# Kernel tuning notes

Hardware: AMD Instinct MI355X
Metric: run time of the kernel (lower is better)

Reference implementation:

```python
import jax, jax.numpy as jnp
import numpy as np

N = 8192
N_DIM = 7
N_WIDTH = 64


def setup_inputs() -> dict:
    key = jax.random.key(0)
    ks = jax.random.split(key, 12)
    scale = 0.05
    u = lambda k, shape: scale * (2.0 * jax.random.uniform(k, shape) - 1.0)
    # Linear params stored as (in, out) so forward uses x @ W + b (same math as torch Linear).
    lin = lambda k, fan_in, fan_out: (
        jax.random.uniform(jax.random.fold_in(k, 0), (fan_in, fan_out),
                           minval=-1.0, maxval=1.0) / np.sqrt(fan_in),
        jax.random.uniform(jax.random.fold_in(k, 1), (fan_out,),
                           minval=-1.0, maxval=1.0) / np.sqrt(fan_in),
    )
    W1, b1 = lin(ks[1], N_DIM, N_WIDTH)
    W2, b2 = lin(ks[2], N_WIDTH, N_WIDTH)
    Wl, bl = lin(ks[3], N_WIDTH, 1)
    return {
        "x": jax.random.normal(ks[0], (N, N_DIM), dtype=jnp.float32),
        "alpha": jax.random.uniform(ks[4], (1,)),          # Edges.alpha = 1 * rand(1)
        "W1": W1, "b1": b1, "wt1": u(ks[5], (N_WIDTH, N_WIDTH)), "bs1": u(ks[6], (1,)),
        "W2": W2, "b2": b2, "wt2": u(ks[7], (N_WIDTH, N_WIDTH)), "bs2": u(ks[8], (1,)),
        "Wl": Wl, "bl": bl,
    }


def _edges(x, alpha):
    eta, phi = x[:, 1], x[:, 2]
    deta = eta[:, None] - eta[None, :]                      # (n, n)
    dphi = jnp.abs(phi[:, None] - phi[None, :])
    dphi = jnp.where(dphi > jnp.pi, 2.0 * jnp.pi - dphi, dphi)
    dRdR = deta * deta + dphi * dphi
    A = jnp.exp(-alpha[0] * dRdR)
    return jax.nn.softmax(A, axis=1) + jnp.eye(x.shape[0], dtype=x.dtype)


def _gcn_layer(X, A, W, b, wt, bs):
    X = jax.nn.relu(X @ W + b)                              # embed + relu
    X = (A @ X) @ wt + bs[0]                                # aggregate + mix + scalar bias
    return jax.nn.relu(X)


def reference(x, alpha, W1, b1, wt1, bs1, W2, b2, wt2, bs2, Wl, bl):
    A = _edges(x, alpha)
    V = jax.nn.relu(_gcn_layer(x, A, W1, b1, wt1, bs1))
    V = jax.nn.relu(_gcn_layer(V, A, W2, b2, wt2, bs2))
    s = V.sum(axis=0)                                       # (n_width,)
    return jax.nn.sigmoid(s @ Wl + bl)                      # (1,)
```

## Files before the change

kernel.cpp:

```cpp
#include <hip/hip_runtime.h>
#include <math.h>

#define NN 8192
#define L2E 1.44269504088896340736f
#define TWO_PI 6.28318530717958647693f

typedef _Float16 h8 __attribute__((ext_vector_type(8)));
typedef _Float16 h4 __attribute__((ext_vector_type(4)));
typedef float f32x4 __attribute__((ext_vector_type(4)));
typedef float f32x2 __attribute__((ext_vector_type(2)));
#define MFMA16(A, B, C) __builtin_amdgcn_mfma_f32_16x16x32_f16(A, B, C, 0, 0, 0)

#define GLD_LDS16(gsrc, ldst)                                          \
  __builtin_amdgcn_global_load_lds(                                    \
      (const __attribute__((address_space(1))) unsigned int*)(gsrc),   \
      (__attribute__((address_space(3))) unsigned int*)(ldst), 16, 0, 0)

union V8 { float4 v[2]; float f[8]; };

__global__ __launch_bounds__(256) void prep_kernel(
    const float* __restrict__ x, const float* __restrict__ alpha,
    const float* __restrict__ W1, const float* __restrict__ b1,
    float* __restrict__ eta_s, float* __restrict__ phi_s,
    float* __restrict__ H1, _Float16* __restrict__ HT1,
    float* __restrict__ svec)
{
  __shared__ float sW[448];
  __shared__ float sb[64];
  __shared__ float T[32][68];
  const int t = threadIdx.x;
  if (blockIdx.x == 0 && t < 64) svec[t] = 0.f;
  for (int k = t; k < 448; k += 256) sW[k] = W1[k];
  if (t < 64) sb[t] = b1[t];
  const float s = sqrtf(alpha[0] * L2E);
  const int i0 = blockIdx.x * 32;
  const int r = t >> 3, q = t & 7;
  const int i = i0 + r;
  float xv[7];
#pragma unroll
  for (int k = 0; k < 7; k++) xv[k] = x[i * 7 + k];
  if (q == 0) { eta_s[i] = xv[1] * s; phi_s[i] = xv[2] * s; }
  __syncthreads();
#pragma unroll
  for (int c = 0; c < 8; c++) {
    const int n = q * 8 + c;
    float hv = sb[n];
#pragma unroll
    for (int k = 0; k < 7; k++) hv = fmaf(xv[k], sW[k * 64 + n], hv);
    T[r][n] = fmaxf(hv, 0.f);
  }
  __syncthreads();
  for (int e = t; e < 512; e += 256)
    *(f32x4*)(H1 + (size_t)i0 * 64 + (e << 2)) =
        *(const f32x4*)&T[e >> 4][(e << 2) & 63];
  const int n = t >> 2, sg = (t & 3) * 8;
  h8 v;
#pragma unroll
  for (int ss = 0; ss < 8; ss++) v[ss] = (_Float16)T[sg + ss][n];
  *(h8*)(HT1 + (size_t)n * NN + i0 + sg) = v;
}

template <bool NEED_L>
__global__ __launch_bounds__(256, 4) void attn_pass(
    const float* __restrict__ eta_s, const float* __restrict__ phi_s,
    const _Float16* __restrict__ HT, const float* __restrict__ alpha,
    float* __restrict__ Ypart, float* __restrict__ lpart)
{
  __shared__ __align__(16) char smem[32768];
  const int tid = threadIdx.x;
  const int w = tid >> 6, lane = tid & 63, m = lane & 15, g = lane >> 4;
  const int tile = blockIdx.x >> 2, part = blockIdx.x & 3;
  const int i0 = tile << 5;
  const int jbase = part << 11;
  const float Cs = TWO_PI * sqrtf(alpha[0] * L2E);
  const float et0 = eta_s[i0 + m],      ph0 = phi_s[i0 + m];
  const float et1 = eta_s[i0 + 16 + m], ph1 = phi_s[i0 + 16 + m];

  const int joff = jbase + (w << 5) + (g << 3);
  const _Float16* hb = HT + (size_t)m * NN + joff;
  const float* ep = eta_s + joff;
  const float* pp = phi_s + joff;

  char* const slab = smem + (w << 13);

  f32x4 a00 = {0,0,0,0}, a01 = {0,0,0,0}, a02 = {0,0,0,0}, a03 = {0,0,0,0};
  f32x4 a10 = {0,0,0,0}, a11 = {0,0,0,0}, a12 = {0,0,0,0}, a13 = {0,0,0,0};
  f32x4 l0a = {0,0,0,0}, l1a = {0,0,0,0};
  const h8 onesv = {(_Float16)1.f, (_Float16)1.f, (_Float16)1.f, (_Float16)1.f,
                    (_Float16)1.f, (_Float16)1.f, (_Float16)1.f, (_Float16)1.f};

  V8 Eb[2], Pb[2];

#pragma unroll
  for (int k = 0; k < 4; ++k)
    GLD_LDS16(hb + (size_t)k * 16 * NN, slab + (k << 10));
  Eb[0].v[0] = *(const float4*)(ep);     Eb[0].v[1] = *(const float4*)(ep + 4);
  Pb[0].v[0] = *(const float4*)(pp);     Pb[0].v[1] = *(const float4*)(pp + 4);
  __builtin_amdgcn_sched_barrier(0);

  union AF { h8 v; decltype(__builtin_amdgcn_cvt_pkrtz(0.f, 0.f)) p[4]; };

#pragma unroll
  for (int s = 0; s < 16; ++s) {
    if (s < 15) {
      char* const nb = slab + (((s + 1) & 1) << 12);
      const _Float16* src = hb + (s + 1) * 128;
#pragma unroll
      for (int k = 0; k < 4; ++k)
        GLD_LDS16(src + (size_t)k * 16 * NN, nb + (k << 10));
      Eb[(s + 1) & 1].v[0] = *(const float4*)(ep + (s + 1) * 128);
      Eb[(s + 1) & 1].v[1] = *(const float4*)(ep + (s + 1) * 128 + 4);
      Pb[(s + 1) & 1].v[0] = *(const float4*)(pp + (s + 1) * 128);
      Pb[(s + 1) & 1].v[1] = *(const float4*)(pp + (s + 1) * 128 + 4);
    }
    __builtin_amdgcn_sched_barrier(0);
    if (s < 15) asm volatile("s_waitcnt vmcnt(8)" ::: "memory");
    else        asm volatile("s_waitcnt vmcnt(0)" ::: "memory");
    __builtin_amdgcn_sched_barrier(0);

    const char* fb = slab + ((s & 1) << 12) + (lane << 4);
    const h8 b0 = *(const h8*)(fb);
    const h8 b1 = *(const h8*)(fb + 1024);
    const h8 b2 = *(const h8*)(fb + 2048);
    const h8 b3 = *(const h8*)(fb + 3072);
    const V8& E = Eb[s & 1];
    const V8& P = Pb[s & 1];

    AF af0, af1;
#pragma unroll
    for (int tt = 0; tt < 8; tt += 2) {
      const f32x2 pj = {P.f[tt], P.f[tt + 1]};
      const f32x2 ej = {E.f[tt], E.f[tt + 1]};
      const f32x2 dp0 = ph0 - pj, dp1 = ph1 - pj;
      const f32x2 ad0 = {fabsf(dp0.x), fabsf(dp0.y)};
      const f32x2 ad1 = {fabsf(dp1.x), fabsf(dp1.y)};
      const f32x2 cm0 = Cs - ad0, cm1 = Cs - ad1;
      const f32x2 wr0 = {fminf(ad0.x, cm0.x), fminf(ad0.y, cm0.y)};
      const f32x2 wr1 = {fminf(ad1.x, cm1.x), fminf(ad1.y, cm1.y)};
      const f32x2 de0 = et0 - ej, de1 = et1 - ej;
      const f32x2 r20 = de0 * de0 + wr0 * wr0;
      const f32x2 r21 = de1 * de1 + wr1 * wr1;
      const f32x2 ax0 = {__builtin_amdgcn_exp2f(-r20.x),
                         __builtin_amdgcn_exp2f(-r20.y)};
      const f32x2 ax1 = {__builtin_amdgcn_exp2f(-r21.x),
                         __builtin_amdgcn_exp2f(-r21.y)};
      const f32x2 ga0 = ax0 * L2E - L2E;
      const f32x2 ga1 = ax1 * L2E - L2E;
      af0.p[tt >> 1] = __builtin_amdgcn_cvt_pkrtz(
          __builtin_amdgcn_exp2f(ga0.x), __builtin_amdgcn_exp2f(ga0.y));
      af1.p[tt >> 1] = __builtin_amdgcn_cvt_pkrtz(
          __builtin_amdgcn_exp2f(ga1.x), __builtin_amdgcn_exp2f(ga1.y));
    }
    a00 = MFMA16(af0.v, b0, a00); a01 = MFMA16(af0.v, b1, a01);
    a02 = MFMA16(af0.v, b2, a02); a03 = MFMA16(af0.v, b3, a03);
    a10 = MFMA16(af1.v, b0, a10); a11 = MFMA16(af1.v, b1, a11);
    a12 = MFMA16(af1.v, b2, a12); a13 = MFMA16(af1.v, b3, a13);
    if constexpr (NEED_L) {
      l0a = MFMA16(af0.v, onesv, l0a);
      l1a = MFMA16(af1.v, onesv, l1a);
    }
  }

  __syncthreads();

  typedef float Red2[32][66];
  Red2* red = (Red2*)smem;
  const int h = w >> 1;
  if ((w & 1) == 0) {
#pragma unroll
    for (int r = 0; r < 4; ++r) {
      red[h][g * 4 + r][m]      = a00[r]; red[h][g * 4 + r][16 + m] = a01[r];
      red[h][g * 4 + r][32 + m] = a02[r]; red[h][g * 4 + r][48 + m] = a03[r];
      red[h][16 + g * 4 + r][m]      = a10[r]; red[h][16 + g * 4 + r][16 + m] = a11[r];
      red[h][16 + g * 4 + r][32 + m] = a12[r]; red[h][16 + g * 4 + r][48 + m] = a13[r];
    }
    if constexpr (NEED_L) {
      if (m == 0) {
#pragma unroll
        for (int r = 0; r < 4; ++r) {
          red[h][g * 4 + r][64]      = l0a[r];
          red[h][16 + g * 4 + r][64] = l1a[r];
        }
      }
    }
  }
  __syncthreads();
  if (w & 1) {
#pragma unroll
    for (int r = 0; r < 4; ++r) {
      red[h][g * 4 + r][m]      += a00[r]; red[h][g * 4 + r][16 + m] += a01[r];
      red[h][g * 4 + r][32 + m] += a02[r]; red[h][g * 4 + r][48 + m] += a03[r];
      red[h][16 + g * 4 + r][m]      += a10[r]; red[h][16 + g * 4 + r][16 + m] += a11[r];
      red[h][16 + g * 4 + r][32 + m] += a12[r]; red[h][16 + g * 4 + r][48 + m] += a13[r];
    }
    if constexpr (NEED_L) {
      if (m == 0) {
#pragma unroll
        for (int r = 0; r < 4; ++r) {
          red[h][g * 4 + r][64]      += l0a[r];
          red[h][16 + g * 4 + r][64] += l1a[r];
        }
      }
    }
  }
  __syncthreads();
#pragma unroll
  for (int k = 0; k < 8; ++k) {
    const int e = tid + k * 256;
    Ypart[((size_t)part * NN + i0 + (e >> 6)) * 64 + (e & 63)] =
        red[0][e >> 6][e & 63] + red[1][e >> 6][e & 63];
  }
  if constexpr (NEED_L) {
    if (tid < 32)
      lpart[(size_t)part * NN + i0 + tid] = red[0][tid][64] + red[1][tid][64];
  }
}

__global__ __launch_bounds__(256) void mid_kernel(
    const float* __restrict__ Yp, const float* __restrict__ lp,
    const float* __restrict__ H1, const float* __restrict__ wt1,
    const float* __restrict__ bs1, const float* __restrict__ W2,
    const float* __restrict__ b2, float* __restrict__ H2,
    _Float16* __restrict__ HT2)
{
  __shared__ float sA[64][68];
  __shared__ float sB[64][68];
  __shared__ float U[16][68];
  __shared__ float sb2v[64];
  const int t = threadIdx.x;
  for (int e = t; e < 1024; e += 256) {
    const int rr = e >> 4, cc = (e << 2) & 63;
    *(f32x4*)&sA[rr][cc] = *(const f32x4*)(wt1 + (e << 2));
    *(f32x4*)&sB[rr][cc] = *(const f32x4*)(W2 + (e << 2));
  }
  if (t < 64) sb2v[t] = b2[t];
  const float bsv = bs1[0];
  const int i0 = blockIdx.x * 16;
  const int r = t >> 4, q = t & 15;
  const int i = i0 + r;
  float l = 0.f;
#pragma unroll
  for (int p = 0; p < 4; ++p) l += lp[(size_t)p * NN + i];
  const float rl = 1.0f / l;
  f32x4 ya = {0, 0, 0, 0};
#pragma unroll
  for (int p = 0; p < 4; ++p)
    ya += *(const f32x4*)(Yp + ((size_t)p * NN + i) * 64 + q * 4);
  const f32x4 h1 = *(const f32x4*)(H1 + (size_t)i * 64 + q * 4);
#pragma unroll
  for (int c = 0; c < 4; ++c) U[r][q * 4 + c] = fmaf(ya[c], rl, h1[c]);
  __syncthreads();
  float z[4];
#pragma unroll
  for (int c = 0; c < 4; ++c) z[c] = bsv;
#pragma unroll
  for (int k4 = 0; k4 < 64; k4 += 4) {
    const f32x4 u4 = *(const f32x4*)&U[r][k4];
#pragma unroll
    for (int kk = 0; kk < 4; ++kk) {
      const f32x4 sa = *(const f32x4*)&sA[k4 + kk][q * 4];
#pragma unroll
      for (int c = 0; c < 4; ++c) z[c] = fmaf(u4[kk], sa[c], z[c]);
    }
  }
  __syncthreads();
#pragma unroll
  for (int c = 0; c < 4; ++c) U[r][q * 4 + c] = fmaxf(z[c], 0.f);
  __syncthreads();
  float hv[4];
#pragma unroll
  for (int c = 0; c < 4; ++c) hv[c] = sb2v[q * 4 + c];
#pragma unroll
  for (int k4 = 0; k4 < 64; k4 += 4) {
    const f32x4 u4 = *(const f32x4*)&U[r][k4];
#pragma unroll
    for (int kk = 0; kk < 4; ++kk) {
      const f32x4 sb4 = *(const f32x4*)&sB[k4 + kk][q * 4];
#pragma unroll
      for (int c = 0; c < 4; ++c) hv[c] = fmaf(u4[kk], sb4[c], hv[c]);
    }
  }
  __syncthreads();
#pragma unroll
  for (int c = 0; c < 4; ++c) U[r][q * 4 + c] = fmaxf(hv[c], 0.f);
  __syncthreads();
  *(f32x4*)(H2 + (size_t)i0 * 64 + (t << 2)) =
      *(const f32x4*)&U[t >> 4][(t << 2) & 63];
  const int n = t >> 2, sg = (t & 3) * 4;
  h4 v;
#pragma unroll
  for (int ss = 0; ss < 4; ss++) v[ss] = (_Float16)U[sg + ss][n];
  *(h4*)(HT2 + (size_t)n * NN + i0 + sg) = v;
}

__global__ __launch_bounds__(256) void final_kernel(
    const float* __restrict__ Yp, const float* __restrict__ lp,
    const float* __restrict__ H2, const float* __restrict__ wt2,
    const float* __restrict__ bs2, float* __restrict__ svec)
{
  __shared__ float sA[64][68];
  __shared__ float U[16][68];
  __shared__ float cred[4][64];
  const int t = threadIdx.x;
  for (int e = t; e < 1024; e += 256) {
    const int rr = e >> 4, cc = (e << 2) & 63;
    *(f32x4*)&sA[rr][cc] = *(const f32x4*)(wt2 + (e << 2));
  }
  const float bsv = bs2[0];
  const int i0 = blockIdx.x * 16;
  const int r = t >> 4, q = t & 15;
  const int i = i0 + r;
  float l = 0.f;
#pragma unroll
  for (int p = 0; p < 4; ++p) l += lp[(size_t)p * NN + i];
  const float rl = 1.0f / l;
  f32x4 ya = {0, 0, 0, 0};
#pragma unroll
  for (int p = 0; p < 4; ++p)
    ya += *(const f32x4*)(Yp + ((size_t)p * NN + i) * 64 + q * 4);
  const f32x4 h2 = *(const f32x4*)(H2 + (size_t)i * 64 + q * 4);
#pragma unroll
  for (int c = 0; c < 4; ++c) U[r][q * 4 + c] = fmaf(ya[c], rl, h2[c]);
  __syncthreads();
  float z[4];
#pragma unroll
  for (int c = 0; c < 4; ++c) z[c] = bsv;
#pragma unroll
  for (int k4 = 0; k4 < 64; k4 += 4) {
    const f32x4 u4 = *(const f32x4*)&U[r][k4];
#pragma unroll
    for (int kk = 0; kk < 4; ++kk) {
      const f32x4 sa = *(const f32x4*)&sA[k4 + kk][q * 4];
#pragma unroll
      for (int c = 0; c < 4; ++c) z[c] = fmaf(u4[kk], sa[c], z[c]);
    }
  }
  __syncthreads();
#pragma unroll
  for (int c = 0; c < 4; ++c) U[r][q * 4 + c] = fmaxf(z[c], 0.f);
  __syncthreads();
  const int col = t & 63, rg = t >> 6;
  float ps = 0.f;
#pragma unroll
  for (int rr = 0; rr < 4; rr++) ps += U[rg * 4 + rr][col];
  cred[rg][col] = ps;
  __syncthreads();
  if (t < 64)
    atomicAdd(svec + t, cred[0][t] + cred[1][t] + cred[2][t] + cred[3][t]);
}

__global__ void out_kernel(const float* __restrict__ svec,
                           const float* __restrict__ Wl,
                           const float* __restrict__ bl,
                           float* __restrict__ out)
{
  const int t = threadIdx.x;
  float v = svec[t] * Wl[t];
#pragma unroll
  for (int off = 32; off > 0; off >>= 1) v += __shfl_down(v, off);
  if (t == 0) {
    const float logit = v + bl[0];
    out[0] = 1.0f / (1.0f + __builtin_amdgcn_exp2f(-logit * L2E));
  }
}

extern "C" void kernel_launch(void* const* d_in, const int* in_sizes, int n_in,
                              void* d_out, int out_size, void* d_ws,
                              size_t ws_size, hipStream_t stream)
{
  const float* x     = (const float*)d_in[0];
  const float* alpha = (const float*)d_in[1];
  const float* W1    = (const float*)d_in[2];
  const float* b1    = (const float*)d_in[3];
  const float* wt1   = (const float*)d_in[4];
  const float* bs1   = (const float*)d_in[5];
  const float* W2    = (const float*)d_in[6];
  const float* b2    = (const float*)d_in[7];
  const float* wt2   = (const float*)d_in[8];
  const float* bs2   = (const float*)d_in[9];
  const float* Wl    = (const float*)d_in[10];
  const float* bl    = (const float*)d_in[11];
  float* out = (float*)d_out;

  char* ws = (char*)d_ws;
  size_t off = 0;
  auto alloc = [&](size_t bytes) {
    void* p = ws + off;
    off = (off + bytes + 255) & ~(size_t)255;
    return p;
  };
  float* eta_s = (float*)alloc(NN * 4 + 256);
  float* phi_s = (float*)alloc(NN * 4 + 256);
  float* H1    = (float*)alloc((size_t)NN * 64 * 4);
  float* H2    = (float*)alloc((size_t)NN * 64 * 4);
  float* Ypart = (float*)alloc((size_t)4 * NN * 64 * 4);
  float* lpart = (float*)alloc((size_t)4 * NN * 4);
  _Float16* HT = (_Float16*)alloc((size_t)NN * 64 * 2 + 512);
  float* svec  = (float*)alloc(64 * 4);

  prep_kernel<<<256, 256, 0, stream>>>(x, alpha, W1, b1, eta_s, phi_s, H1, HT, svec);
  attn_pass<true><<<1024, 256, 0, stream>>>(eta_s, phi_s, HT, alpha, Ypart, lpart);
  mid_kernel<<<512, 256, 0, stream>>>(Ypart, lpart, H1, wt1, bs1, W2, b2, H2, HT);
  attn_pass<false><<<1024, 256, 0, stream>>>(eta_s, phi_s, HT, alpha, Ypart, nullptr);
  final_kernel<<<512, 256, 0, stream>>>(Ypart, lpart, H2, wt2, bs2, svec);
  out_kernel<<<1, 64, 0, stream>>>(svec, Wl, bl, out);
}
```

Measured before the change: 193.4 us.

## Split attention j-range into 8 parts and stage eta/phi in LDS

The attention pass now splits the j dimension into 8 partitions instead of 4, doubling the grid to 2048 blocks and halving each block's loop to 8 steps. Each block preloads its eta/phi slice into shared memory once rather than streaming it through registers per step, which reduces vector-memory waits and register pressure. A waves_per_eu hint is added. The cost is twice as many partial Y/l buffers for the mid and final kernels to read and sum, and more LDS per block.

```diff
diff --git a/kernel.cpp b/kernel.cpp
--- a/kernel.cpp
+++ b/kernel.cpp
@@ -61,27 +61,29 @@
 }
 
 template <bool NEED_L>
-__global__ __launch_bounds__(256, 4) void attn_pass(
+__global__ __launch_bounds__(256, 4)
+__attribute__((amdgpu_waves_per_eu(4, 4))) void attn_pass(
     const float* __restrict__ eta_s, const float* __restrict__ phi_s,
     const _Float16* __restrict__ HT, const float* __restrict__ alpha,
     float* __restrict__ Ypart, float* __restrict__ lpart)
 {
-  __shared__ __align__(16) char smem[32768];
+  __shared__ __align__(16) char smem[40960];
+  float* const eL = (float*)smem;
+  float* const pL = (float*)(smem + 4096);
   const int tid = threadIdx.x;
   const int w = tid >> 6, lane = tid & 63, m = lane & 15, g = lane >> 4;
-  const int tile = blockIdx.x >> 2, part = blockIdx.x & 3;
+  const int tile = blockIdx.x >> 3, part = blockIdx.x & 7;
   const int i0 = tile << 5;
-  const int jbase = part << 11;
+  const int jbase = part << 10;
   const float Cs = TWO_PI * sqrtf(alpha[0] * L2E);
   const float et0 = eta_s[i0 + m],      ph0 = phi_s[i0 + m];
   const float et1 = eta_s[i0 + 16 + m], ph1 = phi_s[i0 + 16 + m];
 
-  const int joff = jbase + (w << 5) + (g << 3);
-  const _Float16* hb = HT + (size_t)m * NN + joff;
-  const float* ep = eta_s + joff;
-  const float* pp = phi_s + joff;
-
-  char* const slab = smem + (w << 13);
+  *(f32x4*)&eL[tid * 4] = *(const f32x4*)(eta_s + jbase + tid * 4);
+  *(f32x4*)&pL[tid * 4] = *(const f32x4*)(phi_s + jbase + tid * 4);
+
+  const _Float16* hb = HT + (size_t)m * NN + jbase + (w << 5) + (g << 3);
+  char* const slab = smem + 8192 + (w << 13);
 
   f32x4 a00 = {0,0,0,0}, a01 = {0,0,0,0}, a02 = {0,0,0,0}, a03 = {0,0,0,0};
   f32x4 a10 = {0,0,0,0}, a11 = {0,0,0,0}, a12 = {0,0,0,0}, a13 = {0,0,0,0};
@@ -89,42 +91,35 @@
   const h8 onesv = {(_Float16)1.f, (_Float16)1.f, (_Float16)1.f, (_Float16)1.f,
                     (_Float16)1.f, (_Float16)1.f, (_Float16)1.f, (_Float16)1.f};
 
-  V8 Eb[2], Pb[2];
+  __syncthreads();
 
 #pragma unroll
   for (int k = 0; k < 4; ++k)
     GLD_LDS16(hb + (size_t)k * 16 * NN, slab + (k << 10));
-  Eb[0].v[0] = *(const float4*)(ep);     Eb[0].v[1] = *(const float4*)(ep + 4);
-  Pb[0].v[0] = *(const float4*)(pp);     Pb[0].v[1] = *(const float4*)(pp + 4);
-  __builtin_amdgcn_sched_barrier(0);
 
   union AF { h8 v; decltype(__builtin_amdgcn_cvt_pkrtz(0.f, 0.f)) p[4]; };
 
 #pragma unroll
-  for (int s = 0; s < 16; ++s) {
-    if (s < 15) {
+  for (int s = 0; s < 8; ++s) {
+    if (s < 7) {
       char* const nb = slab + (((s + 1) & 1) << 12);
       const _Float16* src = hb + (s + 1) * 128;
 #pragma unroll
       for (int k = 0; k < 4; ++k)
         GLD_LDS16(src + (size_t)k * 16 * NN, nb + (k << 10));
-      Eb[(s + 1) & 1].v[0] = *(const float4*)(ep + (s + 1) * 128);
-      Eb[(s + 1) & 1].v[1] = *(const float4*)(ep + (s + 1) * 128 + 4);
-      Pb[(s + 1) & 1].v[0] = *(const float4*)(pp + (s + 1) * 128);
-      Pb[(s + 1) & 1].v[1] = *(const float4*)(pp + (s + 1) * 128 + 4);
-    }
-    __builtin_amdgcn_sched_barrier(0);
-    if (s < 15) asm volatile("s_waitcnt vmcnt(8)" ::: "memory");
-    else        asm volatile("s_waitcnt vmcnt(0)" ::: "memory");
-    __builtin_amdgcn_sched_barrier(0);
+    }
+    if (s < 7) asm volatile("s_waitcnt vmcnt(4)" ::: "memory");
+    else       asm volatile("s_waitcnt vmcnt(0)" ::: "memory");
 
     const char* fb = slab + ((s & 1) << 12) + (lane << 4);
     const h8 b0 = *(const h8*)(fb);
     const h8 b1 = *(const h8*)(fb + 1024);
     const h8 b2 = *(const h8*)(fb + 2048);
     const h8 b3 = *(const h8*)(fb + 3072);
-    const V8& E = Eb[s & 1];
-    const V8& P = Pb[s & 1];
+    const int o = s * 128 + (w << 5) + (g << 3);
+    V8 E, P;
+    E.v[0] = *(const float4*)&eL[o]; E.v[1] = *(const float4*)&eL[o + 4];
+    P.v[0] = *(const float4*)&pL[o]; P.v[1] = *(const float4*)&pL[o + 4];
 
     AF af0, af1;
 #pragma unroll
@@ -240,11 +235,11 @@
   const int i = i0 + r;
   float l = 0.f;
 #pragma unroll
-  for (int p = 0; p < 4; ++p) l += lp[(size_t)p * NN + i];
+  for (int p = 0; p < 8; ++p) l += lp[(size_t)p * NN + i];
   const float rl = 1.0f / l;
   f32x4 ya = {0, 0, 0, 0};
 #pragma unroll
-  for (int p = 0; p < 4; ++p)
+  for (int p = 0; p < 8; ++p)
     ya += *(const f32x4*)(Yp + ((size_t)p * NN + i) * 64 + q * 4);
   const f32x4 h1 = *(const f32x4*)(H1 + (size_t)i * 64 + q * 4);
 #pragma unroll
@@ -312,11 +307,11 @@
   const int i = i0 + r;
   float l = 0.f;
 #pragma unroll
-  for (int p = 0; p < 4; ++p) l += lp[(size_t)p * NN + i];
+  for (int p = 0; p < 8; ++p) l += lp[(size_t)p * NN + i];
   const float rl = 1.0f / l;
   f32x4 ya = {0, 0, 0, 0};
 #pragma unroll
-  for (int p = 0; p < 4; ++p)
+  for (int p = 0; p < 8; ++p)
     ya += *(const f32x4*)(Yp + ((size_t)p * NN + i) * 64 + q * 4);
   const f32x4 h2 = *(const f32x4*)(H2 + (size_t)i * 64 + q * 4);
 #pragma unroll
@@ -393,15 +388,15 @@
   float* phi_s = (float*)alloc(NN * 4 + 256);
   float* H1    = (float*)alloc((size_t)NN * 64 * 4);
   float* H2    = (float*)alloc((size_t)NN * 64 * 4);
-  float* Ypart = (float*)alloc((size_t)4 * NN * 64 * 4);
-  float* lpart = (float*)alloc((size_t)4 * NN * 4);
+  float* Ypart = (float*)alloc((size_t)8 * NN * 64 * 4);
+  float* lpart = (float*)alloc((size_t)8 * NN * 4);
   _Float16* HT = (_Float16*)alloc((size_t)NN * 64 * 2 + 512);
   float* svec  = (float*)alloc(64 * 4);
 
   prep_kernel<<<256, 256, 0, stream>>>(x, alpha, W1, b1, eta_s, phi_s, H1, HT, svec);
-  attn_pass<true><<<1024, 256, 0, stream>>>(eta_s, phi_s, HT, alpha, Ypart, lpart);
+  attn_pass<true><<<2048, 256, 0, stream>>>(eta_s, phi_s, HT, alpha, Ypart, lpart);
   mid_kernel<<<512, 256, 0, stream>>>(Ypart, lpart, H1, wt1, bs1, W2, b2, H2, HT);
-  attn_pass<false><<<1024, 256, 0, stream>>>(eta_s, phi_s, HT, alpha, Ypart, nullptr);
+  attn_pass<false><<<2048, 256, 0, stream>>>(eta_s, phi_s, HT, alpha, Ypart, nullptr);
   final_kernel<<<512, 256, 0, stream>>>(Ypart, lpart, H2, wt2, bs2, svec);
   out_kernel<<<1, 64, 0, stream>>>(svec, Wl, bl, out);
 }
```

Result: faster. 185.7 us (-4.0%).
